# Performance work log

Hardware: AMD Instinct MI355X
Metric: run time of the kernel (lower is better)

Reference implementation:

```python
import jax, jax.numpy as jnp
import numpy as np

N = 8192
D = 512


def setup_inputs() -> dict:
    key = jax.random.key(0)
    ks = jax.random.split(key, 6)
    s = 1.0 / np.sqrt(D)
    return {
        "x": jax.random.normal(ks[0], (N, D), jnp.float32),
        "spatial_encoding": jax.random.normal(ks[1], (N, N), jnp.float32),
        "edge_encoding": jax.random.normal(ks[2], (N, N), jnp.float32),
        "Wq": jax.random.normal(ks[3], (D, D), jnp.float32) * s,
        "bq": jnp.zeros((D,), jnp.float32),
        "Wk": jax.random.normal(ks[4], (D, D), jnp.float32) * s,
        "bk": jnp.zeros((D,), jnp.float32),
        "Wv": jax.random.normal(ks[5], (D, D), jnp.float32) * s,
        "bv": jnp.zeros((D,), jnp.float32),
    }


def reference(x, spatial_encoding, edge_encoding, Wq, bq, Wk, bk, Wv, bv):
    # Linear layers (torch nn.Linear: y = x @ W.T + b)
    q = x @ Wq.T + bq  # [N, D]
    k = x @ Wk.T + bk  # [N, D]
    v = x @ Wv.T + bv  # [N, D]
    scale = 1.0 / jnp.sqrt(jnp.asarray(q.shape[-1], q.dtype))
    a = (q @ k.T) * scale + spatial_encoding + edge_encoding  # [N, N]
    attn = jax.nn.softmax(a, axis=-1)
    return attn @ v  # [N, D]
```

## Files before the change

### kernel.cpp

```cpp
#include <hip/hip_runtime.h>


constexpr int NT = 8192;
constexpr int DM = 512;
constexpr float SM_SHIFT = 12.0f;
constexpr float QSCALE = 0.04419417382415922f;

typedef _Float16 f16;
typedef _Float16 half8  __attribute__((ext_vector_type(8)));
typedef _Float16 half4v __attribute__((ext_vector_type(4)));
typedef float    float4v __attribute__((ext_vector_type(4)));

__device__ __forceinline__ void gload_lds16(const void* gsrc, void* ldst) {
  __builtin_amdgcn_global_load_lds(
      (const __attribute__((address_space(1))) void*)gsrc,
      (__attribute__((address_space(3))) void*)ldst, 16, 0, 0);
}

template<int ROWS>
__device__ __forceinline__ void stage32(const f16* __restrict__ g, int ldg,
                                        f16* l, int tid) {
  constexpr int ITERS = (ROWS * 4) / 256;
  #pragma unroll
  for (int c = 0; c < ITERS; ++c) {
    int lin = c * 256 + tid;
    gload_lds16(g + (size_t)(lin >> 2) * ldg + (lin & 3) * 8, l + lin * 8);
  }
}

__global__ __launch_bounds__(256) void k0_convert(
    const float* __restrict__ x, const float* __restrict__ wq,
    const float* __restrict__ wk, const float* __restrict__ wv,
    f16* __restrict__ xh, f16* __restrict__ wh) {
  int i = (blockIdx.x * 256 + threadIdx.x) * 4;
  const float* src; f16* dst; int off;
  if (i < NT * DM) { src = x; dst = xh; off = i; }
  else {
    int t = i - NT * DM;
    int w = t >> 18;
    off = t & ((1 << 18) - 1);
    src = (w == 0) ? wq : (w == 1) ? wk : wv;
    dst = wh + ((size_t)w << 18);
  }
  float4v v = *(const float4v*)(src + off);
  half4v h = { (f16)v.x, (f16)v.y, (f16)v.z, (f16)v.w };
  *(half4v*)(dst + off) = h;
}

__global__ __launch_bounds__(256) void k1_qkv(
    const f16* __restrict__ xh, const f16* __restrict__ wh,
    const float* __restrict__ bq, const float* __restrict__ bk,
    const float* __restrict__ bv,
    f16* __restrict__ qh, f16* __restrict__ kh, f16* __restrict__ vh) {
  __shared__ f16 As[128 * 32], Bs[128 * 32];
  int tid = threadIdx.x;
  int z = blockIdx.z;
  const f16* B0 = wh + (size_t)z * DM * DM;
  const float* bias = (z == 0) ? bq : (z == 1) ? bk : bv;
  f16* outp = (z == 0) ? qh : (z == 1) ? kh : vh;
  float scale = (z == 0) ? QSCALE : 1.0f;
  int i0 = blockIdx.y * 128, j0 = blockIdx.x * 128;
  int lane = tid & 63, warp = tid >> 6;
  int l15 = lane & 15, quad = lane >> 4;
  int wm = (warp >> 1) * 64, wn = (warp & 1) * 64;

  float4v acc[4][4] = {};
  const f16* Ag = xh + (size_t)i0 * DM;
  const f16* Bg = B0 + (size_t)j0 * DM;
  for (int kk = 0; kk < DM; kk += 32) {
    stage32<128>(Ag + kk, DM, As, tid);
    stage32<128>(Bg + kk, DM, Bs, tid);
    __syncthreads();
    half8 a[4], b[4];
    #pragma unroll
    for (int f = 0; f < 4; ++f)
      a[f] = *(const half8*)&As[(wm + f * 16 + l15) * 32 + quad * 8];
    #pragma unroll
    for (int f = 0; f < 4; ++f)
      b[f] = *(const half8*)&Bs[(wn + f * 16 + l15) * 32 + quad * 8];
    #pragma unroll
    for (int fm = 0; fm < 4; ++fm)
      #pragma unroll
      for (int fn = 0; fn < 4; ++fn)
        acc[fm][fn] = __builtin_amdgcn_mfma_f32_16x16x32_f16(
            a[fm], b[fn], acc[fm][fn], 0, 0, 0);
    __syncthreads();
  }
  #pragma unroll
  for (int fm = 0; fm < 4; ++fm)
    #pragma unroll
    for (int r = 0; r < 4; ++r) {
      int grow = i0 + wm + fm * 16 + quad * 4 + r;
      #pragma unroll
      for (int fn = 0; fn < 4; ++fn) {
        int gcol = j0 + wn + fn * 16 + l15;
        float v = (acc[fm][fn][r] + bias[gcol]) * scale;
        outp[(size_t)grow * DM + gcol] = (f16)v;
      }
    }
}

__global__ __launch_bounds__(256) void k15_transpose(
    const f16* __restrict__ v, f16* __restrict__ vT) {
  __shared__ f16 t[64][65];
  int bj = blockIdx.x * 64;
  int bi = blockIdx.y * 64;
  int tx = threadIdx.x & 63, ty = threadIdx.x >> 6;
  #pragma unroll
  for (int i = 0; i < 16; ++i)
    t[ty + i * 4][tx] = v[(size_t)(bi + ty + i * 4) * DM + bj + tx];
  __syncthreads();
  #pragma unroll
  for (int i = 0; i < 16; ++i)
    vT[(size_t)(bj + ty + i * 4) * NT + bi + tx] = t[tx][ty + i * 4];
}

template<bool P16>
__global__ __launch_bounds__(256) void k2_scores(
    const f16* __restrict__ qh, const f16* __restrict__ kh,
    const float* __restrict__ spatial, const float* edge,
    f16* pOut16, float* pOut32, float* __restrict__ rowsum) {
  __shared__ f16 As[128 * 32], Bs[128 * 32];
  int tid = threadIdx.x;
  int i0 = blockIdx.y * 128, j0 = blockIdx.x * 128;
  int lane = tid & 63, warp = tid >> 6;
  int l15 = lane & 15, quad = lane >> 4;
  int wm = (warp >> 1) * 64, wn = (warp & 1) * 64;

  float4v acc[4][4] = {};
  const f16* Ag = qh + (size_t)i0 * DM;
  const f16* Bg = kh + (size_t)j0 * DM;
  for (int kk = 0; kk < DM; kk += 32) {
    stage32<128>(Ag + kk, DM, As, tid);
    stage32<128>(Bg + kk, DM, Bs, tid);
    __syncthreads();
    half8 a[4], b[4];
    #pragma unroll
    for (int f = 0; f < 4; ++f)
      a[f] = *(const half8*)&As[(wm + f * 16 + l15) * 32 + quad * 8];
    #pragma unroll
    for (int f = 0; f < 4; ++f)
      b[f] = *(const half8*)&Bs[(wn + f * 16 + l15) * 32 + quad * 8];
    #pragma unroll
    for (int fm = 0; fm < 4; ++fm)
      #pragma unroll
      for (int fn = 0; fn < 4; ++fn)
        acc[fm][fn] = __builtin_amdgcn_mfma_f32_16x16x32_f16(
            a[fm], b[fn], acc[fm][fn], 0, 0, 0);
    __syncthreads();
  }
  #pragma unroll
  for (int fm = 0; fm < 4; ++fm)
    #pragma unroll
    for (int r = 0; r < 4; ++r) {
      int grow = i0 + wm + fm * 16 + quad * 4 + r;
      float s = 0.f;
      #pragma unroll
      for (int fn = 0; fn < 4; ++fn) {
        int gcol = j0 + wn + fn * 16 + l15;
        size_t idx = (size_t)grow * NT + gcol;
        float lg = acc[fm][fn][r] + spatial[idx] + edge[idx] - SM_SHIFT;
        float p = __expf(lg);
        s += p;
        if (P16) pOut16[idx] = (f16)p;
        else     pOut32[idx] = p;
      }
      s += __shfl_xor(s, 1);
      s += __shfl_xor(s, 2);
      s += __shfl_xor(s, 4);
      s += __shfl_xor(s, 8);
      if (l15 == 0) atomicAdd(&rowsum[grow], s);
    }
}

template<bool P16>
__global__ __launch_bounds__(256) void k3_out(
    const f16* __restrict__ p16, const float* p32,
    const f16* __restrict__ vT, const float* __restrict__ rowsum,
    float* __restrict__ out) {
  __shared__ f16 As[64 * 32], Bs[128 * 32];
  int tid = threadIdx.x;
  int i0 = blockIdx.y * 64;
  int j0 = blockIdx.x * 128;
  int lane = tid & 63, warp = tid >> 6;
  int l15 = lane & 15, quad = lane >> 4;
  int wn = warp * 32;

  float4v acc[4][2] = {};
  const f16* Bg = vT + (size_t)j0 * NT;
  for (int kk = 0; kk < NT; kk += 32) {
    if (P16) {
      stage32<64>(p16 + (size_t)i0 * NT + kk, NT, As, tid);
    } else {
      int row = tid >> 2, cc = tid & 3;
      const float4v* src =
          (const float4v*)(p32 + (size_t)(i0 + row) * NT + kk + cc * 8);
      float4v f0 = src[0], f1 = src[1];
      half8 h = { (f16)f0.x, (f16)f0.y, (f16)f0.z, (f16)f0.w,
                  (f16)f1.x, (f16)f1.y, (f16)f1.z, (f16)f1.w };
      *(half8*)&As[tid * 8] = h;
    }
    stage32<128>(Bg + kk, NT, Bs, tid);
    __syncthreads();
    half8 a[4], b[2];
    #pragma unroll
    for (int f = 0; f < 4; ++f)
      a[f] = *(const half8*)&As[(f * 16 + l15) * 32 + quad * 8];
    #pragma unroll
    for (int f = 0; f < 2; ++f)
      b[f] = *(const half8*)&Bs[(wn + f * 16 + l15) * 32 + quad * 8];
    #pragma unroll
    for (int fm = 0; fm < 4; ++fm)
      #pragma unroll
      for (int fn = 0; fn < 2; ++fn)
        acc[fm][fn] = __builtin_amdgcn_mfma_f32_16x16x32_f16(
            a[fm], b[fn], acc[fm][fn], 0, 0, 0);
    __syncthreads();
  }
  #pragma unroll
  for (int fm = 0; fm < 4; ++fm)
    #pragma unroll
    for (int r = 0; r < 4; ++r) {
      int grow = i0 + fm * 16 + quad * 4 + r;
      float inv = 1.0f / rowsum[grow];
      #pragma unroll
      for (int fn = 0; fn < 2; ++fn) {
        int gcol = j0 + wn + fn * 16 + l15;
        out[(size_t)grow * DM + gcol] = acc[fm][fn][r] * inv;
      }
    }
}

extern "C" void kernel_launch(void* const* d_in, const int* in_sizes, int n_in,
                              void* d_out, int out_size, void* d_ws,
                              size_t ws_size, hipStream_t stream) {
  (void)in_sizes; (void)n_in; (void)out_size;
  const float* x  = (const float*)d_in[0];
  const float* sp = (const float*)d_in[1];
  float*       eg = (float*)d_in[2];
  const float* Wq = (const float*)d_in[3];
  const float* bq = (const float*)d_in[4];
  const float* Wk = (const float*)d_in[5];
  const float* bk = (const float*)d_in[6];
  const float* Wv = (const float*)d_in[7];
  const float* bv = (const float*)d_in[8];
  float* out = (float*)d_out;

  char* ws = (char*)d_ws;
  const size_t MB = 1ull << 20;
  f16* qh = (f16*)(ws + 0 * MB);
  f16* kh = (f16*)(ws + 8 * MB);
  f16* vh = (f16*)(ws + 16 * MB);
  f16* vT = (f16*)(ws + 24 * MB);
  f16* xh = (f16*)(ws + 32 * MB);
  f16* wh = (f16*)(ws + 40 * MB);
  float* rowsum = (float*)(ws + 42 * MB);
  f16* p16 = (f16*)(ws + 48 * MB);
  bool useP16 = ws_size >= 176 * MB;

  k0_convert<<<4864, 256, 0, stream>>>(x, Wq, Wk, Wv, xh, wh);
  (void)hipMemsetAsync(rowsum, 0, NT * sizeof(float), stream);
  k1_qkv<<<dim3(4, 64, 3), 256, 0, stream>>>(xh, wh, bq, bk, bv, qh, kh, vh);
  k15_transpose<<<dim3(8, 128), 256, 0, stream>>>(vh, vT);
  if (useP16) {
    k2_scores<true><<<dim3(64, 64), 256, 0, stream>>>(qh, kh, sp, eg, p16,
                                                      nullptr, rowsum);
    k3_out<true><<<dim3(4, 128), 256, 0, stream>>>(p16, nullptr, vT, rowsum,
                                                   out);
  } else {
    k2_scores<false><<<dim3(64, 64), 256, 0, stream>>>(qh, kh, sp, eg, nullptr,
                                                       eg, rowsum);
    k3_out<false><<<dim3(4, 128), 256, 0, stream>>>(nullptr, eg, vT, rowsum,
                                                    out);
  }
}
```

Before: 800.6 us.

## Stage score tile through LDS for coalesced epilogue; double K-step in output GEMM

```diff
diff --git a/kernel.cpp b/kernel.cpp
--- a/kernel.cpp
+++ b/kernel.cpp
@@ -115,12 +115,18 @@
     vT[(size_t)(bj + ty + i * 4) * NT + bi + tx] = t[tx][ty + i * 4];
 }
 
+constexpr int SLD = 132;
+
 template<bool P16>
 __global__ __launch_bounds__(256) void k2_scores(
     const f16* __restrict__ qh, const f16* __restrict__ kh,
     const float* __restrict__ spatial, const float* edge,
     f16* pOut16, float* pOut32, float* __restrict__ rowsum) {
-  __shared__ f16 As[128 * 32], Bs[128 * 32];
+  __shared__ __align__(16) char smem[32 * SLD * 4];
+  f16* As = (f16*)smem;
+  f16* Bs = (f16*)(smem + 8192);
+  float* slab = (float*)smem;
+
   int tid = threadIdx.x;
   int i0 = blockIdx.y * 128, j0 = blockIdx.x * 128;
   int lane = tid & 63, warp = tid >> 6;
@@ -149,28 +155,67 @@
             a[fm], b[fn], acc[fm][fn], 0, 0, 0);
     __syncthreads();
   }
-  #pragma unroll
-  for (int fm = 0; fm < 4; ++fm)
-    #pragma unroll
-    for (int r = 0; r < 4; ++r) {
-      int grow = i0 + wm + fm * 16 + quad * 4 + r;
-      float s = 0.f;
-      #pragma unroll
-      for (int fn = 0; fn < 4; ++fn) {
-        int gcol = j0 + wn + fn * 16 + l15;
-        size_t idx = (size_t)grow * NT + gcol;
-        float lg = acc[fm][fn][r] + spatial[idx] + edge[idx] - SM_SHIFT;
-        float p = __expf(lg);
-        s += p;
-        if (P16) pOut16[idx] = (f16)p;
-        else     pOut32[idx] = p;
-      }
-      s += __shfl_xor(s, 1);
-      s += __shfl_xor(s, 2);
-      s += __shfl_xor(s, 4);
-      s += __shfl_xor(s, 8);
-      if (l15 == 0) atomicAdd(&rowsum[grow], s);
-    }
+
+  int rrow = tid >> 3;
+  int col0 = (tid & 7) * 16;
+  #pragma unroll
+  for (int s = 0; s < 4; ++s) {
+    if ((warp >> 1) == (s >> 1)) {
+      int fmb = (s & 1) * 2;
+      #pragma unroll
+      for (int f = 0; f < 2; ++f)
+        #pragma unroll
+        for (int r = 0; r < 4; ++r) {
+          int ris = f * 16 + quad * 4 + r;
+          #pragma unroll
+          for (int fn = 0; fn < 4; ++fn)
+            slab[ris * SLD + wn + fn * 16 + l15] = acc[fmb + f][fn][r];
+        }
+    }
+    __syncthreads();
+    {
+      int grow = i0 + s * 32 + rrow;
+      size_t base = (size_t)grow * NT + j0 + col0;
+      float4v sc[4], spv[4], egv[4];
+      #pragma unroll
+      for (int c = 0; c < 4; ++c) {
+        sc[c]  = *(float4v*)&slab[rrow * SLD + col0 + c * 4];
+        spv[c] = *(const float4v*)(spatial + base + c * 4);
+        egv[c] = *(const float4v*)(edge + base + c * 4);
+      }
+      float rs = 0.f;
+      if (P16) {
+        half8 h[2];
+        #pragma unroll
+        for (int c = 0; c < 4; ++c)
+          #pragma unroll
+          for (int e = 0; e < 4; ++e) {
+            float p = __expf(sc[c][e] + spv[c][e] + egv[c][e] - SM_SHIFT);
+            rs += p;
+            h[c >> 1][(c & 1) * 4 + e] = (f16)p;
+          }
+        *(half8*)(pOut16 + base) = h[0];
+        *(half8*)(pOut16 + base + 8) = h[1];
+      } else {
+        #pragma unroll
+        for (int c = 0; c < 4; ++c) {
+          float4v pv;
+          #pragma unroll
+          for (int e = 0; e < 4; ++e) {
+            float p = __expf(sc[c][e] + spv[c][e] + egv[c][e] - SM_SHIFT);
+            rs += p;
+            pv[e] = p;
+          }
+          *(float4v*)(pOut32 + base + c * 4) = pv;
+        }
+      }
+      rs += __shfl_xor(rs, 1);
+      rs += __shfl_xor(rs, 2);
+      rs += __shfl_xor(rs, 4);
+      if ((tid & 7) == 0) atomicAdd(&rowsum[grow], rs);
+    }
+    __syncthreads();
+  }
 }
 
 template<bool P16>
@@ -178,7 +223,7 @@
     const f16* __restrict__ p16, const float* p32,
     const f16* __restrict__ vT, const float* __restrict__ rowsum,
     float* __restrict__ out) {
-  __shared__ f16 As[64 * 32], Bs[128 * 32];
+  __shared__ f16 As[2 * 64 * 32], Bs[2 * 128 * 32];
   int tid = threadIdx.x;
   int i0 = blockIdx.y * 64;
   int j0 = blockIdx.x * 128;
@@ -188,33 +233,42 @@
 
   float4v acc[4][2] = {};
   const f16* Bg = vT + (size_t)j0 * NT;
-  for (int kk = 0; kk < NT; kk += 32) {
+  for (int kk = 0; kk < NT; kk += 64) {
     if (P16) {
       stage32<64>(p16 + (size_t)i0 * NT + kk, NT, As, tid);
+      stage32<64>(p16 + (size_t)i0 * NT + kk + 32, NT, As + 64 * 32, tid);
     } else {
-      int row = tid >> 2, cc = tid & 3;
-      const float4v* src =
-          (const float4v*)(p32 + (size_t)(i0 + row) * NT + kk + cc * 8);
-      float4v f0 = src[0], f1 = src[1];
-      half8 h = { (f16)f0.x, (f16)f0.y, (f16)f0.z, (f16)f0.w,
-                  (f16)f1.x, (f16)f1.y, (f16)f1.z, (f16)f1.w };
-      *(half8*)&As[tid * 8] = h;
+      #pragma unroll
+      for (int sub = 0; sub < 2; ++sub) {
+        int row = tid >> 2, cc = tid & 3;
+        const float4v* src = (const float4v*)(
+            p32 + (size_t)(i0 + row) * NT + kk + sub * 32 + cc * 8);
+        float4v f0 = src[0], f1 = src[1];
+        half8 h = { (f16)f0.x, (f16)f0.y, (f16)f0.z, (f16)f0.w,
+                    (f16)f1.x, (f16)f1.y, (f16)f1.z, (f16)f1.w };
+        *(half8*)&As[sub * 64 * 32 + tid * 8] = h;
+      }
     }
     stage32<128>(Bg + kk, NT, Bs, tid);
-    __syncthreads();
-    half8 a[4], b[2];
-    #pragma unroll
-    for (int f = 0; f < 4; ++f)
-      a[f] = *(const half8*)&As[(f * 16 + l15) * 32 + quad * 8];
-    #pragma unroll
-    for (int f = 0; f < 2; ++f)
-      b[f] = *(const half8*)&Bs[(wn + f * 16 + l15) * 32 + quad * 8];
-    #pragma unroll
-    for (int fm = 0; fm < 4; ++fm)
-      #pragma unroll
-      for (int fn = 0; fn < 2; ++fn)
-        acc[fm][fn] = __builtin_amdgcn_mfma_f32_16x16x32_f16(
-            a[fm], b[fn], acc[fm][fn], 0, 0, 0);
+    stage32<128>(Bg + kk + 32, NT, Bs + 128 * 32, tid);
+    __syncthreads();
+    #pragma unroll
+    for (int sub = 0; sub < 2; ++sub) {
+      half8 a[4], b[2];
+      #pragma unroll
+      for (int f = 0; f < 4; ++f)
+        a[f] = *(const half8*)&As[sub * 2048 + (f * 16 + l15) * 32 + quad * 8];
+      #pragma unroll
+      for (int f = 0; f < 2; ++f)
+        b[f] = *(const half8*)
+            &Bs[sub * 4096 + (wn + f * 16 + l15) * 32 + quad * 8];
+      #pragma unroll
+      for (int fm = 0; fm < 4; ++fm)
+        #pragma unroll
+        for (int fn = 0; fn < 2; ++fn)
+          acc[fm][fn] = __builtin_amdgcn_mfma_f32_16x16x32_f16(
+              a[fm], b[fn], acc[fm][fn], 0, 0, 0);
+    }
     __syncthreads();
   }
   #pragma unroll
```

Measured after the change: 778.0 us. 1.03x faster.
